# Optimization experiments

Hardware: AMD Instinct MI355X
Metric: run time of the kernel (lower is better)

The kernel has to match this reference:

```python
import jax, jax.numpy as jnp
import numpy as np

N = 100000
E = 1600000
D_IN = 128   # encode_dim
D_H = 32     # hidden_dim
R = 2        # num_relations
EPS = 1e-5
NEG_SLOPE = 0.2


def _glorot(k, shape):
    lim = np.sqrt(6.0 / (shape[-2] + shape[-1]))
    return jax.random.uniform(k, shape, jnp.float32, -lim, lim)


def setup_inputs() -> dict:
    key = jax.random.key(0)
    ks = jax.random.split(key, 16)
    inp = {}
    inp['x'] = jax.random.normal(ks[0], (N, D_IN), jnp.float32)
    inp['edge_index'] = jax.random.randint(ks[1], (2, E), 0, N)
    inp['edge_type'] = jax.random.randint(ks[2], (E,), 0, R)
    dims = [D_IN, D_H, D_H]
    i = 3
    for li, din in enumerate(dims):
        inp[f'w{li}'] = _glorot(ks[i], (R, din, D_H)); i += 1
        inp[f'aq{li}'] = _glorot(ks[i], (R, D_H, 1)); i += 1
        inp[f'ak{li}'] = _glorot(ks[i], (R, D_H, 1)); i += 1
        inp[f'b{li}'] = jnp.zeros((D_H,), jnp.float32)
        inp[f'g{li}'] = jnp.ones((D_H,), jnp.float32)
        inp[f'be{li}'] = jnp.zeros((D_H,), jnp.float32)
    inp['mw1'] = _glorot(ks[i], (D_H, D_H)); i += 1
    inp['mb1'] = jnp.zeros((D_H,), jnp.float32)
    inp['mw2'] = _glorot(ks[i], (D_H, 2)); i += 1
    inp['mb2'] = jnp.zeros((2,), jnp.float32)
    return inp


def _rgat(x, src, dst, edge_type, W, Q, K, b):
    """PyG RGATConv, heads=1, additive self-attention, across-relation softmax."""
    n = x.shape[0]
    We = W[edge_type]                              # [E, din, dh]
    xi = jnp.einsum('ed,edh->eh', x[dst], We)      # transformed target feats
    xj = jnp.einsum('ed,edh->eh', x[src], We)      # transformed source feats
    q = jnp.einsum('eh,eho->eo', xi, Q[edge_type])[:, 0]   # [E]
    k = jnp.einsum('eh,eho->eo', xj, K[edge_type])[:, 0]   # [E]
    e = jax.nn.leaky_relu(q + k, NEG_SLOPE)
    # softmax over incoming edges of each destination node
    m = jax.ops.segment_max(e, dst, num_segments=n)
    ex = jnp.exp(e - m[dst])
    s = jax.ops.segment_sum(ex, dst, num_segments=n)
    alpha = ex / (s[dst] + 1e-16)
    out = jax.ops.segment_sum(xj * alpha[:, None], dst, num_segments=n)
    return out + b


def _bn(h, gamma, beta):
    mu = jnp.mean(h, axis=0)
    var = jnp.mean((h - mu) ** 2, axis=0)
    return gamma * (h - mu) * jax.lax.rsqrt(var + EPS) + beta


def reference(x, edge_index, edge_type,
              w0, aq0, ak0, b0, g0, be0,
              w1, aq1, ak1, b1, g1, be1,
              w2, aq2, ak2, b2, g2, be2,
              mw1, mb1, mw2, mb2):
    src, dst = edge_index[0], edge_index[1]
    h = _bn(jax.nn.relu(_rgat(x, src, dst, edge_type, w0, aq0, ak0, b0)), g0, be0)
    h = _bn(jax.nn.relu(_rgat(h, src, dst, edge_type, w1, aq1, ak1, b1)), g1, be1)
    h = _bn(jax.nn.relu(_rgat(h, src, dst, edge_type, w2, aq2, ak2, b2)), g2, be2)
    h = jax.nn.sigmoid(h @ mw1 + mb1)
    out = h @ mw2 + mb2   # [N, 2] logits
    return out
```

## Files before the change

### kernel.cpp

```cpp
#include <hip/hip_runtime.h>
#include <math.h>

#define N_NODES 100000
#define N_EDGES 1600000
#define DIN 128
#define DH 32
#define NEG_SLOPE 0.2f
#define BN_EPS 1e-5f
#define MT 64
#define BSHIFT 9
#define NBUCK 196
#define B_SCAT 256
#define CPB ((N_EDGES + B_SCAT - 1) / B_SCAT)
#define WCONV_ELEMS (64 * DIN + 128 * DH)
#define WCONV_BLOCKS ((WCONV_ELEMS + 255) / 256)

typedef __attribute__((ext_vector_type(8))) short short8;
typedef __attribute__((ext_vector_type(4))) float f32x4;

__device__ __forceinline__ unsigned short f2bf(float f) {
    unsigned int u = __float_as_uint(f);
    u = (u + 0x7FFFu + ((u >> 16) & 1u)) >> 16;
    return (unsigned short)u;
}
__device__ __forceinline__ float bf2f(unsigned short h) {
    return __uint_as_float((unsigned int)h << 16);
}
__device__ __forceinline__ unsigned short f2h(float f) {
    _Float16 hv = (_Float16)f;
    return __builtin_bit_cast(unsigned short, hv);
}
__device__ __forceinline__ float h2f(unsigned short h) {
    return (float)__builtin_bit_cast(_Float16, h);
}


template<int K, bool FUSE_BN>
__device__ __forceinline__ void transform_body(
    const float* __restrict__ xin, const float* __restrict__ stats,
    const float* __restrict__ gamma, const float* __restrict__ beta,
    const unsigned short* __restrict__ WtHi, const unsigned short* __restrict__ WtLo,
    const float* __restrict__ Qw, const float* __restrict__ Kw,
    unsigned short* __restrict__ yb, float* __restrict__ qv, float* __restrict__ kv,
    int tile, int n) {
    constexpr int LDK = K + 8;
    constexpr int KT = K / 32;
    __shared__ unsigned short xs_hi[MT * LDK];
    __shared__ unsigned short xs_lo[MT * LDK];
    __shared__ float scs[DH], shs[DH];
    int tid = threadIdx.x;
    int base = tile * MT;

    if (FUSE_BN) {
        if (tid < DH) {
            float mu = stats[tid] * (1.f / N_NODES);
            float var = stats[DH + tid] * (1.f / N_NODES) - mu * mu;
            float inv = rsqrtf(var + BN_EPS);
            float sc = gamma[tid] * inv;
            scs[tid] = sc;
            shs[tid] = beta[tid] - mu * sc;
        }
        __syncthreads();
    }

    constexpr int CH = K / 4;
    for (int c = tid; c < MT * CH; c += 256) {
        int row = c / CH, c4 = c % CH;
        int node = base + row;
        float4 v = make_float4(0.f, 0.f, 0.f, 0.f);
        if (node < n) v = ((const float4*)(xin + (size_t)node * K))[c4];
        if (FUSE_BN) {
            int c0 = c4 * 4;
            v.x = v.x * scs[c0 + 0] + shs[c0 + 0];
            v.y = v.y * scs[c0 + 1] + shs[c0 + 1];
            v.z = v.z * scs[c0 + 2] + shs[c0 + 2];
            v.w = v.w * scs[c0 + 3] + shs[c0 + 3];
        }
        ushort4 hb = make_ushort4(f2bf(v.x), f2bf(v.y), f2bf(v.z), f2bf(v.w));
        ushort4 lb = make_ushort4(f2bf(v.x - bf2f(hb.x)), f2bf(v.y - bf2f(hb.y)),
                                  f2bf(v.z - bf2f(hb.z)), f2bf(v.w - bf2f(hb.w)));
        *(ushort4*)(&xs_hi[row * LDK + c4 * 4]) = hb;
        *(ushort4*)(&xs_lo[row * LDK + c4 * 4]) = lb;
    }
    __syncthreads();

    int lane = tid & 63;
    int wave = tid >> 6;
    int r16 = lane & 15, g = lane >> 4;
    int wrow = wave * 16;

    f32x4 acc[4];
#pragma unroll
    for (int nt = 0; nt < 4; ++nt) acc[nt] = f32x4{0.f, 0.f, 0.f, 0.f};

#pragma unroll
    for (int kt = 0; kt < KT; ++kt) {
        short8 a_hi = *(const short8*)(&xs_hi[(wrow + r16) * LDK + kt * 32 + g * 8]);
        short8 a_lo = *(const short8*)(&xs_lo[(wrow + r16) * LDK + kt * 32 + g * 8]);
#pragma unroll
        for (int nt = 0; nt < 4; ++nt) {
            const size_t bo = (size_t)(nt * 16 + r16) * K + kt * 32 + g * 8;
            short8 b_hi = *(const short8*)(WtHi + bo);
            short8 b_lo = *(const short8*)(WtLo + bo);
            acc[nt] = __builtin_amdgcn_mfma_f32_16x16x32_bf16(a_hi, b_hi, acc[nt], 0, 0, 0);
            acc[nt] = __builtin_amdgcn_mfma_f32_16x16x32_bf16(a_hi, b_lo, acc[nt], 0, 0, 0);
            acc[nt] = __builtin_amdgcn_mfma_f32_16x16x32_bf16(a_lo, b_hi, acc[nt], 0, 0, 0);
        }
    }

    float qp[2][4] = {{0.f, 0.f, 0.f, 0.f}, {0.f, 0.f, 0.f, 0.f}};
    float kp[2][4] = {{0.f, 0.f, 0.f, 0.f}, {0.f, 0.f, 0.f, 0.f}};
#pragma unroll
    for (int nt = 0; nt < 4; ++nt) {
        int col = nt * 16 + r16;
        int rr = col >> 5, cc = col & 31;
        float qw = Qw[rr * DH + cc], kw = Kw[rr * DH + cc];
#pragma unroll
        for (int j = 0; j < 4; ++j) {
            float v = acc[nt][j];
            qp[rr][j] += v * qw;
            kp[rr][j] += v * kw;
            int node = base + wrow + g * 4 + j;
            if (node < n) yb[(size_t)node * 64 + col] = f2h(v);
        }
    }
#pragma unroll
    for (int j = 0; j < 4; ++j) {
#pragma unroll
        for (int rr = 0; rr < 2; ++rr) {
            float q = qp[rr][j], k = kp[rr][j];
            for (int d = 8; d; d >>= 1) {
                q += __shfl_xor(q, d, 16);
                k += __shfl_xor(k, d, 16);
            }
            if (r16 == 0) {
                int node = base + wrow + g * 4 + j;
                if (node < n) {
                    qv[node * 2 + rr] = q;
                    kv[node * 2 + rr] = k;
                }
            }
        }
    }
}


__global__ __launch_bounds__(256) void hist_wconv_kernel(
    const int* __restrict__ dst, int* __restrict__ bh, int e,
    const float* __restrict__ w0, unsigned short* __restrict__ wt0h, unsigned short* __restrict__ wt0l,
    const float* __restrict__ w1, unsigned short* __restrict__ wt1h, unsigned short* __restrict__ wt1l,
    const float* __restrict__ w2, unsigned short* __restrict__ wt2h, unsigned short* __restrict__ wt2l,
    float* __restrict__ stats) {
    if (blockIdx.x < B_SCAT) {
        __shared__ int lh[NBUCK];
        for (int j = threadIdx.x; j < NBUCK; j += 256) lh[j] = 0;
        __syncthreads();
        int b = blockIdx.x;
        int lo = b * CPB, hi = min(lo + CPB, e);
        for (int i = lo + threadIdx.x; i < hi; i += 256)
            atomicAdd(&lh[dst[i] >> BSHIFT], 1);
        __syncthreads();
        for (int j = threadIdx.x; j < NBUCK; j += 256) bh[j * B_SCAT + b] = lh[j];
    } else {
        int i = (blockIdx.x - B_SCAT) * 256 + threadIdx.x;
        if (blockIdx.x == B_SCAT && threadIdx.x < 3 * 2 * DH) stats[threadIdx.x] = 0.f;
        const float* w;
        unsigned short *wh, *wl;
        int K, idx;
        if (i < 64 * DIN) { w = w0; wh = wt0h; wl = wt0l; K = DIN; idx = i; }
        else if (i < 64 * DIN + 64 * DH) { w = w1; wh = wt1h; wl = wt1l; K = DH; idx = i - 64 * DIN; }
        else if (i < 64 * DIN + 128 * DH) { w = w2; wh = wt2h; wl = wt2l; K = DH; idx = i - 64 * DIN - 64 * DH; }
        else return;
        int col = idx / K, k = idx % K;
        int r = col >> 5, c = col & 31;
        float v = w[(r * K + k) * DH + c];
        unsigned short h = f2bf(v);
        wh[idx] = h;
        wl[idx] = f2bf(v - bf2f(h));
    }
}


__global__ __launch_bounds__(1024) void bucket_scan_kernel(
    const int* __restrict__ bh, int* __restrict__ bs, int total) {
    __shared__ int part[1024];
    int t = threadIdx.x;
    int chunk = (total + 1023) >> 10;
    int lo = t * chunk, hi = min(lo + chunk, total);
    int s = 0;
    for (int i = lo; i < hi; ++i) s += bh[i];
    part[t] = s;
    __syncthreads();
    for (int d = 1; d < 1024; d <<= 1) {
        int v = (t >= d) ? part[t - d] : 0;
        __syncthreads();
        part[t] += v;
        __syncthreads();
    }
    int run = t ? part[t - 1] : 0;
    for (int i = lo; i < hi; ++i) { int v = bh[i]; bs[i] = run; run += v; }
}


__global__ __launch_bounds__(256) void scatter_transform0_kernel(
    const int* __restrict__ src, const int* __restrict__ dst, const int* __restrict__ et,
    const int* __restrict__ bs, int* __restrict__ rec, int e,
    const float* __restrict__ x,
    const unsigned short* __restrict__ WtHi, const unsigned short* __restrict__ WtLo,
    const float* __restrict__ Qw, const float* __restrict__ Kw,
    unsigned short* __restrict__ yb, float* __restrict__ qv, float* __restrict__ kv, int n) {
    if (blockIdx.x < B_SCAT) {
        __shared__ int cur[NBUCK];
        int b = blockIdx.x;
        for (int j = threadIdx.x; j < NBUCK; j += 256) cur[j] = bs[j * B_SCAT + b];
        __syncthreads();
        int lo = b * CPB, hi = min(lo + CPB, e);
        for (int i = lo + threadIdx.x; i < hi; i += 256) {
            int d = dst[i];
            int pos = atomicAdd(&cur[d >> BSHIFT], 1);
            rec[pos] = ((d & ((1 << BSHIFT) - 1)) << 18) | (src[i] << 1) | et[i];
        }
    } else {
        transform_body<DIN, false>(x, nullptr, nullptr, nullptr, WtHi, WtLo,
                                   Qw, Kw, yb, qv, kv, (int)blockIdx.x - B_SCAT, n);
    }
}


__global__ __launch_bounds__(256) void fine_scatter_kernel(
    const int* __restrict__ rec, const int* __restrict__ bs,
    int* __restrict__ off, int* __restrict__ packed, int n, int e) {
    __shared__ int ldeg[1 << BSHIFT];
    __shared__ int lpos[1 << BSHIFT];
    int k = blockIdx.x, t = threadIdx.x;
    int nb0 = k << BSHIFT;
    ldeg[t] = 0;
    ldeg[t + 256] = 0;
    __syncthreads();
    int start = bs[k * B_SCAT];
    int end = (k + 1 < NBUCK) ? bs[(k + 1) * B_SCAT] : e;
    for (int i = start + t; i < end; i += 256)
        atomicAdd(&ldeg[rec[i] >> 18], 1);
    __syncthreads();
    lpos[t] = ldeg[t];
    lpos[t + 256] = ldeg[t + 256];
    __syncthreads();
    for (int d = 1; d < (1 << BSHIFT); d <<= 1) {
        int v0 = (t >= d) ? lpos[t - d] : 0;
        int v1 = (t + 256 >= d) ? lpos[t + 256 - d] : 0;
        __syncthreads();
        lpos[t] += v0;
        lpos[t + 256] += v1;
        __syncthreads();
    }
    int e0 = lpos[t] - ldeg[t];
    int e1 = lpos[t + 256] - ldeg[t + 256];
    __syncthreads();
    lpos[t] = start + e0;
    lpos[t + 256] = start + e1;
    int node0 = nb0 + t, node1 = nb0 + t + 256;
    if (node0 < n) off[node0] = start + e0;
    if (node1 < n) off[node1] = start + e1;
    if (k == 0 && t == 0) off[n] = e;
    __syncthreads();
    for (int i = start + t; i < end; i += 256) {
        int r = rec[i];
        int pos = atomicAdd(&lpos[r >> 18], 1);
        packed[pos] = r & 0x3FFFF;
    }
}


template<int K>
__global__ __launch_bounds__(256) void transform_h_kernel(
    const float* __restrict__ xin, const float* __restrict__ stats,
    const float* __restrict__ gamma, const float* __restrict__ beta,
    const unsigned short* __restrict__ WtHi, const unsigned short* __restrict__ WtLo,
    const float* __restrict__ Qw, const float* __restrict__ Kw,
    unsigned short* __restrict__ yb, float* __restrict__ qv, float* __restrict__ kv, int n) {
    transform_body<K, true>(xin, stats, gamma, beta, WtHi, WtLo, Qw, Kw,
                            yb, qv, kv, blockIdx.x, n);
}


__global__ __launch_bounds__(256) void attn_kernel(
    const int* __restrict__ off, const int* __restrict__ packed,
    const unsigned short* __restrict__ y, const float* __restrict__ qv,
    const float* __restrict__ kv, const float* __restrict__ bias,
    float* __restrict__ hpre, float* __restrict__ stats, int n) {
    __shared__ float ssum[DH], ssq[DH];
    if (threadIdx.x < DH) { ssum[threadIdx.x] = 0.f; ssq[threadIdx.x] = 0.f; }
    __syncthreads();
    int lane = threadIdx.x & 31;
    int sub = threadIdx.x >> 5;
    int spb = blockDim.x >> 5;
    float rsum = 0.f, rsq = 0.f;
    float bl = bias[lane];
    for (int node = blockIdx.x * spb + sub; node < n; node += gridDim.x * spb) {
        int lo = off[node], hi = off[node + 1];
        float q0 = qv[node * 2], q1 = qv[node * 2 + 1];
        float acc0 = 0.f, acc1 = 0.f, acc2 = 0.f, acc3 = 0.f, wsum = 0.f;
        for (int base = lo; base < hi; base += 32) {
            int i = base + lane;
            float w = 0.f;
            int row = 0;
            if (i < hi) {
                int p = __builtin_nontemporal_load(packed + i);
                float ev = ((p & 1) ? q1 : q0) + kv[p];
                ev = ev > 0.f ? ev : NEG_SLOPE * ev;
                w = __expf(ev - 8.f);
                row = p << 5;
            }
            wsum += w;
            int cnt = min(32, hi - base);
            int j = 0;
            for (; j + 4 <= cnt; j += 4) {
                float w0 = __shfl(w, j, 32),     w1 = __shfl(w, j + 1, 32);
                float w2 = __shfl(w, j + 2, 32), w3 = __shfl(w, j + 3, 32);
                int r0 = __shfl(row, j, 32),     r1 = __shfl(row, j + 1, 32);
                int r2 = __shfl(row, j + 2, 32), r3 = __shfl(row, j + 3, 32);
                acc0 += w0 * h2f(y[r0 + lane]);
                acc1 += w1 * h2f(y[r1 + lane]);
                acc2 += w2 * h2f(y[r2 + lane]);
                acc3 += w3 * h2f(y[r3 + lane]);
            }
            for (; j < cnt; ++j) {
                float w0 = __shfl(w, j, 32);
                int r0 = __shfl(row, j, 32);
                acc0 += w0 * h2f(y[r0 + lane]);
            }
        }
        for (int d = 16; d; d >>= 1) wsum += __shfl_xor(wsum, d, 32);
        float h = fmaxf((acc0 + acc1 + acc2 + acc3) / (wsum + 1e-16f) + bl, 0.f);
        __builtin_nontemporal_store(h, &hpre[(size_t)node * DH + lane]);
        rsum += h;
        rsq += h * h;
    }
    atomicAdd(&ssum[lane], rsum);
    atomicAdd(&ssq[lane], rsq);
    __syncthreads();
    if (threadIdx.x < DH) {
        atomicAdd(&stats[threadIdx.x], ssum[threadIdx.x]);
        atomicAdd(&stats[DH + threadIdx.x], ssq[threadIdx.x]);
    }
}


__global__ __launch_bounds__(256) void mlp_kernel(
    const float* __restrict__ hpre, const float* __restrict__ stats,
    const float* __restrict__ gamma, const float* __restrict__ beta,
    const float* __restrict__ mw1, const float* __restrict__ mb1,
    const float* __restrict__ mw2, const float* __restrict__ mb2,
    float* __restrict__ out, int n) {
    int g = (blockIdx.x * blockDim.x + threadIdx.x) >> 5;
    int lane = threadIdx.x & 31;
    if (g >= n) return;
    float mu = stats[lane] * (1.f / N_NODES);
    float var = stats[DH + lane] * (1.f / N_NODES) - mu * mu;
    float inv = rsqrtf(var + BN_EPS);
    float h = gamma[lane] * (hpre[(size_t)g * DH + lane] - mu) * inv + beta[lane];
    float a = mb1[lane];
#pragma unroll
    for (int f = 0; f < DH; ++f) a += __shfl(h, f, 32) * mw1[f * DH + lane];
    float s = 1.f / (1.f + __expf(-a));
    float o0 = s * mw2[lane * 2 + 0];
    float o1 = s * mw2[lane * 2 + 1];
    for (int d = 16; d; d >>= 1) {
        o0 += __shfl_xor(o0, d, 32);
        o1 += __shfl_xor(o1, d, 32);
    }
    if (lane == 0) {
        out[(size_t)g * 2 + 0] = o0 + mb2[0];
        out[(size_t)g * 2 + 1] = o1 + mb2[1];
    }
}


extern "C" void kernel_launch(void* const* d_in, const int* in_sizes, int n_in,
                              void* d_out, int out_size, void* d_ws, size_t ws_size,
                              hipStream_t stream) {
    const float* x = (const float*)d_in[0];
    const int* edge_index = (const int*)d_in[1];
    const int* edge_type = (const int*)d_in[2];
    const float* w[3]  = {(const float*)d_in[3],  (const float*)d_in[9],  (const float*)d_in[15]};
    const float* aq[3] = {(const float*)d_in[4],  (const float*)d_in[10], (const float*)d_in[16]};
    const float* ak[3] = {(const float*)d_in[5],  (const float*)d_in[11], (const float*)d_in[17]};
    const float* bb[3] = {(const float*)d_in[6],  (const float*)d_in[12], (const float*)d_in[18]};
    const float* gm[3] = {(const float*)d_in[7],  (const float*)d_in[13], (const float*)d_in[19]};
    const float* be[3] = {(const float*)d_in[8],  (const float*)d_in[14], (const float*)d_in[20]};
    const float* mw1 = (const float*)d_in[21];
    const float* mb1 = (const float*)d_in[22];
    const float* mw2 = (const float*)d_in[23];
    const float* mb2 = (const float*)d_in[24];
    float* out = (float*)d_out;

    const int n = N_NODES, e = N_EDGES;
    char* ws = (char*)d_ws;
    auto alloc = [&](size_t bytes) {
        char* p = ws;
        ws += (bytes + 255) & ~(size_t)255;
        return p;
    };
    int* off      = (int*)alloc((size_t)(n + 1) * 4);
    int* bhist    = (int*)alloc((size_t)NBUCK * B_SCAT * 4);
    int* bscan    = (int*)alloc((size_t)NBUCK * B_SCAT * 4);
    int* rec      = (int*)alloc((size_t)e * 4);
    int* packed   = (int*)alloc((size_t)e * 4);
    unsigned short* yb = (unsigned short*)alloc((size_t)n * 2 * DH * 2);
    float* qv     = (float*)alloc((size_t)n * 2 * 4);
    float* kv     = (float*)alloc((size_t)n * 2 * 4);
    float* hpre   = (float*)alloc((size_t)n * DH * 4);
    float* stats  = (float*)alloc(3 * 2 * DH * 4);
    unsigned short* wt0h = (unsigned short*)alloc((size_t)64 * DIN * 2);
    unsigned short* wt0l = (unsigned short*)alloc((size_t)64 * DIN * 2);
    unsigned short* wt1h = (unsigned short*)alloc((size_t)64 * DH * 2);
    unsigned short* wt1l = (unsigned short*)alloc((size_t)64 * DH * 2);
    unsigned short* wt2h = (unsigned short*)alloc((size_t)64 * DH * 2);
    unsigned short* wt2l = (unsigned short*)alloc((size_t)64 * DH * 2);

    const int* src = edge_index;
    const int* dst = edge_index + e;

    int tblocks = (n + MT - 1) / MT;

    hist_wconv_kernel<<<B_SCAT + WCONV_BLOCKS, 256, 0, stream>>>(
        dst, bhist, e,
        w[0], wt0h, wt0l, w[1], wt1h, wt1l, w[2], wt2h, wt2l, stats);
    bucket_scan_kernel<<<1, 1024, 0, stream>>>(bhist, bscan, NBUCK * B_SCAT);
    scatter_transform0_kernel<<<B_SCAT + tblocks, 256, 0, stream>>>(
        src, dst, edge_type, bscan, rec, e,
        x, wt0h, wt0l, aq[0], ak[0], yb, qv, kv, n);
    fine_scatter_kernel<<<NBUCK, 256, 0, stream>>>(rec, bscan, off, packed, n, e);

    attn_kernel<<<2048, 256, 0, stream>>>(off, packed, yb, qv, kv, bb[0], hpre, stats + 0 * 64, n);

    transform_h_kernel<DH><<<tblocks, 256, 0, stream>>>(
        hpre, stats + 0 * 64, gm[0], be[0], wt1h, wt1l, aq[1], ak[1], yb, qv, kv, n);
    attn_kernel<<<2048, 256, 0, stream>>>(off, packed, yb, qv, kv, bb[1], hpre, stats + 1 * 64, n);

    transform_h_kernel<DH><<<tblocks, 256, 0, stream>>>(
        hpre, stats + 1 * 64, gm[1], be[1], wt2h, wt2l, aq[2], ak[2], yb, qv, kv, n);
    attn_kernel<<<2048, 256, 0, stream>>>(off, packed, yb, qv, kv, bb[2], hpre, stats + 2 * 64, n);

    mlp_kernel<<<((size_t)n * 32 + 255) / 256, 256, 0, stream>>>(
        hpre, stats + 2 * 64, gm[2], be[2], mw1, mb1, mw2, mb2, out, n);
}
```

Baseline: 456.5 us.

## Stage gathered neighbor rows through LDS with per-lane vector loads in attention

Each lane now loads its edge's full 32-element fp16 source row with four 16-byte loads and writes it into a padded per-subgroup LDS tile, then every lane reads its own column across all 32 staged rows. This replaces the shuffle-driven per-element 2-byte global gathers. It aims to cut the number of global memory transactions and shuffle overhead. In exchange it adds LDS traffic, explicit waitcnt/sched barriers, and always processes 32 rows per chunk even when fewer edges remain (inactive lanes load row 0 with zero weight). It relies on a wave of 32-lane sub-groups staying in lockstep, since there is no barrier between the LDS writes and the reads.

```diff
diff --git a/kernel.cpp b/kernel.cpp
--- a/kernel.cpp
+++ b/kernel.cpp
@@ -14,6 +14,8 @@
 #define CPB ((N_EDGES + B_SCAT - 1) / B_SCAT)
 #define WCONV_ELEMS (64 * DIN + 128 * DH)
 #define WCONV_BLOCKS ((WCONV_ELEMS + 255) / 256)
+#define YSTRIDE 36
+#define SUBSTRIDE 1156
 
 typedef __attribute__((ext_vector_type(8))) short short8;
 typedef __attribute__((ext_vector_type(4))) float f32x4;
@@ -289,17 +291,21 @@
     const float* __restrict__ kv, const float* __restrict__ bias,
     float* __restrict__ hpre, float* __restrict__ stats, int n) {
     __shared__ float ssum[DH], ssq[DH];
+    __shared__ unsigned short ylds[8 * SUBSTRIDE];
+    __shared__ float wlds[8][32];
     if (threadIdx.x < DH) { ssum[threadIdx.x] = 0.f; ssq[threadIdx.x] = 0.f; }
     __syncthreads();
     int lane = threadIdx.x & 31;
     int sub = threadIdx.x >> 5;
     int spb = blockDim.x >> 5;
+    unsigned short* ysub = ylds + sub * SUBSTRIDE;
+    unsigned short* ywr = ysub + lane * YSTRIDE;
     float rsum = 0.f, rsq = 0.f;
     float bl = bias[lane];
     for (int node = blockIdx.x * spb + sub; node < n; node += gridDim.x * spb) {
         int lo = off[node], hi = off[node + 1];
         float q0 = qv[node * 2], q1 = qv[node * 2 + 1];
-        float acc0 = 0.f, acc1 = 0.f, acc2 = 0.f, acc3 = 0.f, wsum = 0.f;
+        float acc = 0.f, wsum = 0.f;
         for (int base = lo; base < hi; base += 32) {
             int i = base + lane;
             float w = 0.f;
@@ -312,26 +318,33 @@
                 row = p << 5;
             }
             wsum += w;
-            int cnt = min(32, hi - base);
-            int j = 0;
-            for (; j + 4 <= cnt; j += 4) {
-                float w0 = __shfl(w, j, 32),     w1 = __shfl(w, j + 1, 32);
-                float w2 = __shfl(w, j + 2, 32), w3 = __shfl(w, j + 3, 32);
-                int r0 = __shfl(row, j, 32),     r1 = __shfl(row, j + 1, 32);
-                int r2 = __shfl(row, j + 2, 32), r3 = __shfl(row, j + 3, 32);
-                acc0 += w0 * h2f(y[r0 + lane]);
-                acc1 += w1 * h2f(y[r1 + lane]);
-                acc2 += w2 * h2f(y[r2 + lane]);
-                acc3 += w3 * h2f(y[r3 + lane]);
+            const uint4* yr = (const uint4*)(y + row);
+            uint4 a = yr[0], b = yr[1], c = yr[2], d = yr[3];
+            wlds[sub][lane] = w;
+            ((uint2*)ywr)[0] = ((uint2*)&a)[0];
+            ((uint2*)ywr)[1] = ((uint2*)&a)[1];
+            ((uint2*)ywr)[2] = ((uint2*)&b)[0];
+            ((uint2*)ywr)[3] = ((uint2*)&b)[1];
+            ((uint2*)ywr)[4] = ((uint2*)&c)[0];
+            ((uint2*)ywr)[5] = ((uint2*)&c)[1];
+            ((uint2*)ywr)[6] = ((uint2*)&d)[0];
+            ((uint2*)ywr)[7] = ((uint2*)&d)[1];
+            asm volatile("s_waitcnt lgkmcnt(0)" ::: "memory");
+            __builtin_amdgcn_sched_barrier(0);
+            float a0 = 0.f, a1 = 0.f, a2 = 0.f, a3 = 0.f;
+#pragma unroll
+            for (int e2 = 0; e2 < 32; e2 += 4) {
+                a0 += wlds[sub][e2 + 0] * h2f(ysub[(e2 + 0) * YSTRIDE + lane]);
+                a1 += wlds[sub][e2 + 1] * h2f(ysub[(e2 + 1) * YSTRIDE + lane]);
+                a2 += wlds[sub][e2 + 2] * h2f(ysub[(e2 + 2) * YSTRIDE + lane]);
+                a3 += wlds[sub][e2 + 3] * h2f(ysub[(e2 + 3) * YSTRIDE + lane]);
             }
-            for (; j < cnt; ++j) {
-                float w0 = __shfl(w, j, 32);
-                int r0 = __shfl(row, j, 32);
-                acc0 += w0 * h2f(y[r0 + lane]);
-            }
+            acc += (a0 + a1) + (a2 + a3);
+            asm volatile("s_waitcnt lgkmcnt(0)" ::: "memory");
+            __builtin_amdgcn_sched_barrier(0);
         }
         for (int d = 16; d; d >>= 1) wsum += __shfl_xor(wsum, d, 32);
-        float h = fmaxf((acc0 + acc1 + acc2 + acc3) / (wsum + 1e-16f) + bl, 0.f);
+        float h = fmaxf(acc / (wsum + 1e-16f) + bl, 0.f);
         __builtin_nontemporal_store(h, &hpre[(size_t)node * DH + lane]);
         rsum += h;
         rsq += h * h;
```

Result: faster. 447.2 us (-2.0%).
